# Kernel optimization log

Measured on AMD Instinct MI355X. Metric: run time of the kernel, lower is better.

## Reference

```python
import jax, jax.numpy as jnp
import numpy as np

BN_EPS = 1e-5

def setup_inputs() -> dict:
    key = jax.random.key(0)
    ks = jax.random.split(key, 8)
    N, E, D = 50000, 800000, 128
    x = jax.random.normal(ks[0], (N, D), dtype=jnp.float32)
    edge_index = jax.random.randint(ks[1], (2, E), 0, N, dtype=jnp.int64)
    s = 1.0 / np.sqrt(D)
    W1 = jax.random.uniform(ks[2], (D, D), jnp.float32, -s, s)
    b1 = jax.random.uniform(ks[3], (D,), jnp.float32, -s, s)
    W2 = jax.random.uniform(ks[4], (D, D), jnp.float32, -s, s)
    b2 = jax.random.uniform(ks[5], (D,), jnp.float32, -s, s)
    g1 = jnp.ones((D,), jnp.float32); be1 = jnp.zeros((D,), jnp.float32)
    g2 = jnp.ones((D,), jnp.float32); be2 = jnp.zeros((D,), jnp.float32)
    eps = jnp.zeros((), jnp.float32)  # learnable GIN epsilon (train_eps=True)
    return {"x": x, "edge_index": edge_index, "eps": eps,
            "W1": W1, "b1": b1, "g1": g1, "be1": be1,
            "W2": W2, "b2": b2, "g2": g2, "be2": be2}

def _batchnorm(h, gamma, beta):
    # training-mode BatchNorm1d over node axis (biased variance)
    mu = jnp.mean(h, axis=0)
    var = jnp.mean(jnp.square(h - mu), axis=0)
    return (h - mu) * jax.lax.rsqrt(var + BN_EPS) * gamma + beta

def reference(x, edge_index, eps, W1, b1, g1, be1, W2, b2, g2, be2):
    N = x.shape[0]
    src, dst = edge_index[0], edge_index[1]
    # GIN aggregation: sum of neighbor features (scatter-add to target nodes)
    agg = jax.ops.segment_sum(x[src], dst, num_segments=N)  # [N, D]
    h = (1.0 + eps) * x + agg
    # MLP: Linear -> BN -> ReLU -> Linear
    h = h @ W1.T + b1
    h = jax.nn.relu(_batchnorm(h, g1, be1))
    h = h @ W2.T + b2
    # outer BatchNorm + ReLU
    return jax.nn.relu(_batchnorm(h, g2, be2))
```

## Files before the change

### kernel.cpp

```cpp
#include <hip/hip_runtime.h>
#include <hip/hip_bf16.h>


#define DIM 128
#define SUB 2
#define CAP 32
#define KMAX 64
#define RBLK 2048

typedef unsigned short u16;
typedef __attribute__((ext_vector_type(8))) short short8;
typedef __attribute__((ext_vector_type(8))) unsigned short ushort8;
typedef __attribute__((ext_vector_type(4))) float f32x4;

__device__ inline u16 f2b(float f) {
  unsigned int u = __builtin_bit_cast(unsigned int, f);
  u += 0x7fffu + ((u >> 16) & 1u);
  return (u16)(u >> 16);
}
__device__ inline float b2f(u16 b) {
  unsigned int u = ((unsigned int)b) << 16;
  return __builtin_bit_cast(float, u);
}

__global__ __launch_bounds__(256) void prep_reorder_kernel(
    const float* __restrict__ W1, const float* __restrict__ W2,
    const float* __restrict__ x, const int* __restrict__ ei,
    int* __restrict__ cursor, u16* __restrict__ buckets,
    u16* __restrict__ wb1, u16* __restrict__ wb2, u16* __restrict__ xb,
    int E, float p8N, int CT, int perC) {
  const int bid = blockIdx.x;
  const int phase = (bid >> 3) & 1;

#pragma unroll
  for (int ph = 0; ph < 2; ++ph) {
    if ((ph ^ phase) == 0) {
      const int beg = bid * perC;
      const int end = min(CT, beg + perC);
      for (int i = beg + (int)threadIdx.x; i < end; i += 256) {
        if (i < 4096) {
          const float4 v = reinterpret_cast<const float4*>(W1)[i];
          ushort4 o = {f2b(v.x), f2b(v.y), f2b(v.z), f2b(v.w)};
          reinterpret_cast<ushort4*>(wb1)[i] = o;
        } else if (i < 8192) {
          const int j = i - 4096;
          const float4 v = reinterpret_cast<const float4*>(W2)[j];
          ushort4 o = {f2b(v.x), f2b(v.y), f2b(v.z), f2b(v.w)};
          reinterpret_cast<ushort4*>(wb2)[j] = o;
        } else {
          const int j = i - 8192;
          const float4 v = reinterpret_cast<const float4*>(x)[j];
          ushort4 o = {f2b(v.x), f2b(v.y), f2b(v.z), f2b(v.w)};
          reinterpret_cast<ushort4*>(xb)[j] = o;
        }
      }
    } else {
      const int part = bid & 7;
      const int slice = bid >> 3;
      const int perE = (E + 255) >> 8;
      const int beg = slice * perE;
      const int end = min(E, beg + perE);
      const int way = threadIdx.x & 1;
      for (int e = beg + (int)threadIdx.x; e < end; e += 256) {
        const int d = ei[E + e];
        int p = (int)((float)d * p8N);
        if (p > 7) p = 7;
        if (p != part) continue;
        const int s = ei[e];
        const int pos = atomicAdd(&cursor[d * SUB + way], 1);
        if (pos < CAP) buckets[d * KMAX + way * CAP + pos] = (u16)s;
      }
    }
  }
}

__global__ __launch_bounds__(256) void aggregate_kernel(
    const u16* __restrict__ xb, const int* __restrict__ cursor,
    const u16* __restrict__ buckets, const float* __restrict__ epsp,
    u16* __restrict__ hb, int N) {
  const int wid = threadIdx.x >> 6;
  const int lane = threadIdx.x & 63;
  const int node = blockIdx.x * 4 + wid;
  if (node >= N) return;
  const int slot = lane >> 4;
  const int chunk = lane & 15;
  int c0 = cursor[node * SUB + 0]; if (c0 > CAP) c0 = CAP;
  int c1 = cursor[node * SUB + 1]; if (c1 > CAP) c1 = CAP;
  const int deg = c0 + c1;
  const u16* bk = buckets + node * KMAX;

  int my = 0;
  if (lane < c0) my = bk[lane];
  else if (lane - c0 < c1) my = bk[CAP + lane - c0];

  float acc[8];
#pragma unroll
  for (int f = 0; f < 8; ++f) acc[f] = 0.f;

  for (int t0 = 0; t0 < deg; t0 += 4) {
    const int idx = t0 + slot;
    const int src = __shfl(my, idx);
    const ushort8 v = *reinterpret_cast<const ushort8*>(xb + (size_t)src * DIM + chunk * 8);
    if (idx < deg) {
#pragma unroll
      for (int f = 0; f < 8; ++f) acc[f] += b2f(v[f]);
    }
  }
#pragma unroll
  for (int f = 0; f < 8; ++f) {
    acc[f] += __shfl_xor(acc[f], 16);
    acc[f] += __shfl_xor(acc[f], 32);
  }
  if (slot == 0) {
    const float k = 1.0f + epsp[0];
    const ushort8 xv = *reinterpret_cast<const ushort8*>(xb + (size_t)node * DIM + chunk * 8);
    ushort8 o;
#pragma unroll
    for (int f = 0; f < 8; ++f) o[f] = f2b(acc[f] + k * b2f(xv[f]));
    *reinterpret_cast<ushort8*>(hb + (size_t)node * DIM + chunk * 8) = o;
  }
}

template <int FUSE>
__global__ __launch_bounds__(256) void gemm_mfma_kernel(
    const void* __restrict__ Av, const u16* __restrict__ Wb,
    const float* __restrict__ bias, const float* __restrict__ statsIn,
    const float* __restrict__ gamma, const float* __restrict__ beta,
    void* __restrict__ Cv, float* __restrict__ statsOut, int N, float Ninv) {
  __shared__ float sred[4][DIM];
  __shared__ float qred[4][DIM];
  __shared__ float ssc[DIM];
  __shared__ float ssh[DIM];
  if (FUSE) {
    const int t = threadIdx.x;
    if (t < DIM) {
      const float mu = statsIn[t] * Ninv;
      const float var = statsIn[DIM + t] * Ninv - mu * mu;
      const float sc = gamma[t] * rsqrtf(var + 1e-5f);
      ssc[t] = sc;
      ssh[t] = beta[t] - mu * sc;
    }
    __syncthreads();
  }
  const int lane = threadIdx.x & 63;
  const int wid = threadIdx.x >> 6;
  const int l15 = lane & 15;
  const int lg = lane >> 4;
  const int wrow = blockIdx.x * 64 + wid * 16;

  f32x4 acc[8];
#pragma unroll
  for (int ni = 0; ni < 8; ++ni) acc[ni] = (f32x4){0.f, 0.f, 0.f, 0.f};

  int arow = wrow + l15;
  if (arow >= N) arow = N - 1;

#pragma unroll
  for (int kb = 0; kb < 4; ++kb) {
    const int k0 = kb * 32 + lg * 8;
    short8 a;
    if (FUSE) {
      const float* A = (const float*)Av + (size_t)arow * DIM + k0;
      const float4 v0 = *reinterpret_cast<const float4*>(A);
      const float4 v1 = *reinterpret_cast<const float4*>(A + 4);
      a[0] = (short)f2b(fmaxf(fmaf(v0.x, ssc[k0 + 0], ssh[k0 + 0]), 0.f));
      a[1] = (short)f2b(fmaxf(fmaf(v0.y, ssc[k0 + 1], ssh[k0 + 1]), 0.f));
      a[2] = (short)f2b(fmaxf(fmaf(v0.z, ssc[k0 + 2], ssh[k0 + 2]), 0.f));
      a[3] = (short)f2b(fmaxf(fmaf(v0.w, ssc[k0 + 3], ssh[k0 + 3]), 0.f));
      a[4] = (short)f2b(fmaxf(fmaf(v1.x, ssc[k0 + 4], ssh[k0 + 4]), 0.f));
      a[5] = (short)f2b(fmaxf(fmaf(v1.y, ssc[k0 + 5], ssh[k0 + 5]), 0.f));
      a[6] = (short)f2b(fmaxf(fmaf(v1.z, ssc[k0 + 6], ssh[k0 + 6]), 0.f));
      a[7] = (short)f2b(fmaxf(fmaf(v1.w, ssc[k0 + 7], ssh[k0 + 7]), 0.f));
    } else {
      a = *reinterpret_cast<const short8*>((const u16*)Av + (size_t)arow * DIM + k0);
    }
#pragma unroll
    for (int ni = 0; ni < 8; ++ni) {
      const short8 b = *reinterpret_cast<const short8*>(Wb + (ni * 16 + l15) * DIM + k0);
      acc[ni] = __builtin_amdgcn_mfma_f32_16x16x32_bf16(a, b, acc[ni], 0, 0, 0);
    }
  }

  const int rbase = wrow + lg * 4;
#pragma unroll
  for (int ni = 0; ni < 8; ++ni) {
    const int col = ni * 16 + l15;
    const float bv = bias[col];
    float s = 0.f, q = 0.f;
#pragma unroll
    for (int r = 0; r < 4; ++r) {
      const int row = rbase + r;
      if (row < N) {
        const float v = acc[ni][r] + bv;
        if (FUSE) {
          const u16 bb = f2b(v);
          const float vr = b2f(bb);
          ((u16*)Cv)[(size_t)row * DIM + col] = bb;
          s += vr;
          q = fmaf(vr, vr, q);
        } else {
          ((float*)Cv)[(size_t)row * DIM + col] = v;
          s += v;
          q = fmaf(v, v, q);
        }
      }
    }
    s += __shfl_xor(s, 16); s += __shfl_xor(s, 32);
    q += __shfl_xor(q, 16); q += __shfl_xor(q, 32);
    if (lg == 0) { sred[wid][col] = s; qred[wid][col] = q; }
  }
  __syncthreads();
  const int t = threadIdx.x;
  if (t < DIM) {
    unsafeAtomicAdd(&statsOut[t], sred[0][t] + sred[1][t] + sred[2][t] + sred[3][t]);
  } else {
    const int c = t - DIM;
    unsafeAtomicAdd(&statsOut[DIM + c], qred[0][c] + qred[1][c] + qred[2][c] + qred[3][c]);
  }
}

__global__ __launch_bounds__(256) void bnrelu_kernel(
    const u16* __restrict__ hb, float* __restrict__ out,
    const float* __restrict__ stats, const float* __restrict__ gamma,
    const float* __restrict__ beta, float Ninv, int total8) {
  __shared__ float ssc[DIM];
  __shared__ float ssh[DIM];
  {
    const int t = threadIdx.x;
    if (t < DIM) {
      const float mu = stats[t] * Ninv;
      const float var = stats[DIM + t] * Ninv - mu * mu;
      const float sc = gamma[t] * rsqrtf(var + 1e-5f);
      ssc[t] = sc;
      ssh[t] = beta[t] - mu * sc;
    }
    __syncthreads();
  }
  int i = blockIdx.x * blockDim.x + threadIdx.x;
  const int stride = gridDim.x * blockDim.x;
  for (; i < total8; i += stride) {
    const int c0 = (i * 8) & (DIM - 1);
    const ushort8 v = reinterpret_cast<const ushort8*>(hb)[i];
    float4 o0, o1;
    o0.x = fmaxf(fmaf(b2f(v[0]), ssc[c0 + 0], ssh[c0 + 0]), 0.f);
    o0.y = fmaxf(fmaf(b2f(v[1]), ssc[c0 + 1], ssh[c0 + 1]), 0.f);
    o0.z = fmaxf(fmaf(b2f(v[2]), ssc[c0 + 2], ssh[c0 + 2]), 0.f);
    o0.w = fmaxf(fmaf(b2f(v[3]), ssc[c0 + 3], ssh[c0 + 3]), 0.f);
    o1.x = fmaxf(fmaf(b2f(v[4]), ssc[c0 + 4], ssh[c0 + 4]), 0.f);
    o1.y = fmaxf(fmaf(b2f(v[5]), ssc[c0 + 5], ssh[c0 + 5]), 0.f);
    o1.z = fmaxf(fmaf(b2f(v[6]), ssc[c0 + 6], ssh[c0 + 6]), 0.f);
    o1.w = fmaxf(fmaf(b2f(v[7]), ssc[c0 + 7], ssh[c0 + 7]), 0.f);
    reinterpret_cast<float4*>(out)[i * 2] = o0;
    reinterpret_cast<float4*>(out)[i * 2 + 1] = o1;
  }
}

extern "C" void kernel_launch(void* const* d_in, const int* in_sizes, int n_in,
                              void* d_out, int out_size, void* d_ws, size_t ws_size,
                              hipStream_t stream) {
  const float* x   = (const float*)d_in[0];
  const int*   ei  = (const int*)d_in[1];
  const float* eps = (const float*)d_in[2];
  const float* W1  = (const float*)d_in[3];
  const float* b1  = (const float*)d_in[4];
  const float* g1  = (const float*)d_in[5];
  const float* be1 = (const float*)d_in[6];
  const float* W2  = (const float*)d_in[7];
  const float* b2  = (const float*)d_in[8];
  const float* g2  = (const float*)d_in[9];
  const float* be2 = (const float*)d_in[10];
  float* out = (float*)d_out;

  const int N = in_sizes[0] / DIM;
  const int E = in_sizes[1] / 2;

  u16* hb      = (u16*)d_ws;
  u16* wb1     = hb + (size_t)N * DIM;
  u16* wb2     = wb1 + DIM * DIM;
  u16* buckets = wb2 + DIM * DIM;
  int* cursor  = (int*)(buckets + (size_t)N * KMAX);
  float* stats1 = (float*)(cursor + SUB * N);
  float* stats2 = stats1 + 256;

  u16* xb = (u16*)d_out;

  const int NX = N * DIM / 4;
  const int CT = 8192 + NX;
  const int perC = (CT + RBLK - 1) / RBLK;
  const float Ninv = 1.0f / N;
  const float p8N = 8.0f / N;

  hipMemsetAsync(cursor, 0, (size_t)(SUB * N + 512) * sizeof(int), stream);

  prep_reorder_kernel<<<RBLK, 256, 0, stream>>>(
      W1, W2, x, ei, cursor, buckets, wb1, wb2, xb, E, p8N, CT, perC);

  aggregate_kernel<<<(N + 3) / 4, 256, 0, stream>>>(xb, cursor, buckets, eps, hb, N);

  const int gblocks = (N + 63) / 64;
  gemm_mfma_kernel<0><<<gblocks, 256, 0, stream>>>(
      hb, wb1, b1, nullptr, nullptr, nullptr, (float*)d_out, stats1, N, Ninv);
  gemm_mfma_kernel<1><<<gblocks, 256, 0, stream>>>(
      (float*)d_out, wb2, b2, stats1, g1, be1, hb, stats2, N, Ninv);
  bnrelu_kernel<<<2048, 256, 0, stream>>>(hb, out, stats2, g2, be2, Ninv, N * (DIM / 8));
}
```

Before: 253.8 us.

## Apply W1 before aggregation and overlap first GEMM with edge bucketing

Uses linearity to compute y = x·W1ᵀ first (fused with the x-to-bf16 conversion) and then aggregates y over neighbours, adding bias afterward. This removes the separate x conversion pass and the first GEMM over the aggregated features. The y GEMM blocks share a launch with the edge-bucketing blocks so the two overlap. A separate stats kernel now reads h1 to compute BN1 statistics, and cursor zeroing moves from a memset into a setup kernel. The gather loop is unrolled to two rows per iteration, and nontemporal loads and stores are added. This adds an extra full read of h1 and changes bf16 rounding points.

```diff
diff --git a/kernel.cpp b/kernel.cpp
--- a/kernel.cpp
+++ b/kernel.cpp
@@ -23,61 +23,100 @@
   return __builtin_bit_cast(float, u);
 }
 
-__global__ __launch_bounds__(256) void prep_reorder_kernel(
+__global__ __launch_bounds__(256) void setup_kernel(
     const float* __restrict__ W1, const float* __restrict__ W2,
-    const float* __restrict__ x, const int* __restrict__ ei,
-    int* __restrict__ cursor, u16* __restrict__ buckets,
-    u16* __restrict__ wb1, u16* __restrict__ wb2, u16* __restrict__ xb,
-    int E, float p8N, int CT, int perC) {
+    int* __restrict__ cursor, u16* __restrict__ wb1, u16* __restrict__ wb2, int ZC) {
+  int i = blockIdx.x * 256 + threadIdx.x;
+  const int stride = gridDim.x * 256;
+  const int e1 = ZC + 4096, e2 = ZC + 8192;
+  for (; i < e2; i += stride) {
+    if (i < ZC) {
+      int4 z = {0, 0, 0, 0};
+      reinterpret_cast<int4*>(cursor)[i] = z;
+    } else if (i < e1) {
+      const int j = i - ZC;
+      const float4 v = reinterpret_cast<const float4*>(W1)[j];
+      ushort4 o = {f2b(v.x), f2b(v.y), f2b(v.z), f2b(v.w)};
+      reinterpret_cast<ushort4*>(wb1)[j] = o;
+    } else {
+      const int j = i - e1;
+      const float4 v = reinterpret_cast<const float4*>(W2)[j];
+      ushort4 o = {f2b(v.x), f2b(v.y), f2b(v.z), f2b(v.w)};
+      reinterpret_cast<ushort4*>(wb2)[j] = o;
+    }
+  }
+}
+
+__global__ __launch_bounds__(256) void reorder_gemmy_kernel(
+    const float* __restrict__ x, const int* __restrict__ ei, const u16* __restrict__ wb1,
+    int* __restrict__ cursor, u16* __restrict__ buckets, u16* __restrict__ yb,
+    int E, float p8N, int N, int GB) {
   const int bid = blockIdx.x;
-  const int phase = (bid >> 3) & 1;
-
-#pragma unroll
-  for (int ph = 0; ph < 2; ++ph) {
-    if ((ph ^ phase) == 0) {
-      const int beg = bid * perC;
-      const int end = min(CT, beg + perC);
-      for (int i = beg + (int)threadIdx.x; i < end; i += 256) {
-        if (i < 4096) {
-          const float4 v = reinterpret_cast<const float4*>(W1)[i];
-          ushort4 o = {f2b(v.x), f2b(v.y), f2b(v.z), f2b(v.w)};
-          reinterpret_cast<ushort4*>(wb1)[i] = o;
-        } else if (i < 8192) {
-          const int j = i - 4096;
-          const float4 v = reinterpret_cast<const float4*>(W2)[j];
-          ushort4 o = {f2b(v.x), f2b(v.y), f2b(v.z), f2b(v.w)};
-          reinterpret_cast<ushort4*>(wb2)[j] = o;
-        } else {
-          const int j = i - 8192;
-          const float4 v = reinterpret_cast<const float4*>(x)[j];
-          ushort4 o = {f2b(v.x), f2b(v.y), f2b(v.z), f2b(v.w)};
-          reinterpret_cast<ushort4*>(xb)[j] = o;
-        }
+  if (bid < GB) {
+    const int lane = threadIdx.x & 63;
+    const int wid = threadIdx.x >> 6;
+    const int l15 = lane & 15;
+    const int lg = lane >> 4;
+    const int wrow = bid * 64 + wid * 16;
+
+    f32x4 acc[8];
+#pragma unroll
+    for (int ni = 0; ni < 8; ++ni) acc[ni] = (f32x4){0.f, 0.f, 0.f, 0.f};
+
+    int arow = wrow + l15;
+    if (arow >= N) arow = N - 1;
+
+#pragma unroll
+    for (int kb = 0; kb < 4; ++kb) {
+      const int k0 = kb * 32 + lg * 8;
+      const f32x4* A = reinterpret_cast<const f32x4*>(x + (size_t)arow * DIM + k0);
+      const f32x4 v0 = __builtin_nontemporal_load(A);
+      const f32x4 v1 = __builtin_nontemporal_load(A + 1);
+      short8 a;
+      a[0] = (short)f2b(v0.x); a[1] = (short)f2b(v0.y);
+      a[2] = (short)f2b(v0.z); a[3] = (short)f2b(v0.w);
+      a[4] = (short)f2b(v1.x); a[5] = (short)f2b(v1.y);
+      a[6] = (short)f2b(v1.z); a[7] = (short)f2b(v1.w);
+#pragma unroll
+      for (int ni = 0; ni < 8; ++ni) {
+        const short8 b = *reinterpret_cast<const short8*>(wb1 + (ni * 16 + l15) * DIM + k0);
+        acc[ni] = __builtin_amdgcn_mfma_f32_16x16x32_bf16(a, b, acc[ni], 0, 0, 0);
       }
-    } else {
-      const int part = bid & 7;
-      const int slice = bid >> 3;
-      const int perE = (E + 255) >> 8;
-      const int beg = slice * perE;
-      const int end = min(E, beg + perE);
-      const int way = threadIdx.x & 1;
-      for (int e = beg + (int)threadIdx.x; e < end; e += 256) {
-        const int d = ei[E + e];
-        int p = (int)((float)d * p8N);
-        if (p > 7) p = 7;
-        if (p != part) continue;
-        const int s = ei[e];
-        const int pos = atomicAdd(&cursor[d * SUB + way], 1);
-        if (pos < CAP) buckets[d * KMAX + way * CAP + pos] = (u16)s;
+    }
+    const int rbase = wrow + lg * 4;
+#pragma unroll
+    for (int ni = 0; ni < 8; ++ni) {
+      const int col = ni * 16 + l15;
+#pragma unroll
+      for (int r = 0; r < 4; ++r) {
+        const int row = rbase + r;
+        if (row < N) yb[(size_t)row * DIM + col] = f2b(acc[ni][r]);
       }
     }
+  } else {
+    const int rb = bid - GB;
+    const int part = rb & 7;
+    const int slice = rb >> 3;
+    const int perE = (E + 255) >> 8;
+    const int beg = slice * perE;
+    const int end = min(E, beg + perE);
+    const int way = threadIdx.x & 1;
+    for (int e = beg + (int)threadIdx.x; e < end; e += 256) {
+      const int d = __builtin_nontemporal_load(ei + E + e);
+      int p = (int)((float)d * p8N);
+      if (p > 7) p = 7;
+      if (p != part) continue;
+      const int s = __builtin_nontemporal_load(ei + e);
+      const int pos = atomicAdd(&cursor[d * SUB + way], 1);
+      if (pos < CAP) buckets[d * KMAX + way * CAP + pos] = (u16)s;
+    }
   }
 }
 
 __global__ __launch_bounds__(256) void aggregate_kernel(
-    const u16* __restrict__ xb, const int* __restrict__ cursor,
+    const u16* __restrict__ yb, const int* __restrict__ cursor,
     const u16* __restrict__ buckets, const float* __restrict__ epsp,
-    u16* __restrict__ hb, int N) {
+    const float* __restrict__ b1, float* __restrict__ h1, int N) {
   const int wid = threadIdx.x >> 6;
   const int lane = threadIdx.x & 63;
   const int node = blockIdx.x * 4 + wid;
@@ -97,13 +136,20 @@
 #pragma unroll
   for (int f = 0; f < 8; ++f) acc[f] = 0.f;
 
-  for (int t0 = 0; t0 < deg; t0 += 4) {
-    const int idx = t0 + slot;
-    const int src = __shfl(my, idx);
-    const ushort8 v = *reinterpret_cast<const ushort8*>(xb + (size_t)src * DIM + chunk * 8);
-    if (idx < deg) {
-#pragma unroll
-      for (int f = 0; f < 8; ++f) acc[f] += b2f(v[f]);
+  for (int t0 = 0; t0 < deg; t0 += 8) {
+    const int i1 = t0 + slot;
+    const int i2 = t0 + 4 + slot;
+    const int s1 = __shfl(my, i1);
+    const int s2 = __shfl(my, i2);
+    const ushort8 v1 = *reinterpret_cast<const ushort8*>(yb + (size_t)s1 * DIM + chunk * 8);
+    const ushort8 v2 = *reinterpret_cast<const ushort8*>(yb + (size_t)s2 * DIM + chunk * 8);
+    if (i1 < deg) {
+#pragma unroll
+      for (int f = 0; f < 8; ++f) acc[f] += b2f(v1[f]);
+    }
+    if (i2 < deg) {
+#pragma unroll
+      for (int f = 0; f < 8; ++f) acc[f] += b2f(v2[f]);
     }
   }
 #pragma unroll
@@ -113,25 +159,54 @@
   }
   if (slot == 0) {
     const float k = 1.0f + epsp[0];
-    const ushort8 xv = *reinterpret_cast<const ushort8*>(xb + (size_t)node * DIM + chunk * 8);
-    ushort8 o;
-#pragma unroll
-    for (int f = 0; f < 8; ++f) o[f] = f2b(acc[f] + k * b2f(xv[f]));
-    *reinterpret_cast<ushort8*>(hb + (size_t)node * DIM + chunk * 8) = o;
-  }
-}
-
-template <int FUSE>
-__global__ __launch_bounds__(256) void gemm_mfma_kernel(
-    const void* __restrict__ Av, const u16* __restrict__ Wb,
+    const ushort8 xv = *reinterpret_cast<const ushort8*>(yb + (size_t)node * DIM + chunk * 8);
+    const float4 bb0 = *reinterpret_cast<const float4*>(b1 + chunk * 8);
+    const float4 bb1 = *reinterpret_cast<const float4*>(b1 + chunk * 8 + 4);
+    float4 o0, o1;
+    o0.x = acc[0] + k * b2f(xv[0]) + bb0.x;
+    o0.y = acc[1] + k * b2f(xv[1]) + bb0.y;
+    o0.z = acc[2] + k * b2f(xv[2]) + bb0.z;
+    o0.w = acc[3] + k * b2f(xv[3]) + bb0.w;
+    o1.x = acc[4] + k * b2f(xv[4]) + bb1.x;
+    o1.y = acc[5] + k * b2f(xv[5]) + bb1.y;
+    o1.z = acc[6] + k * b2f(xv[6]) + bb1.z;
+    o1.w = acc[7] + k * b2f(xv[7]) + bb1.w;
+    float4* dst = reinterpret_cast<float4*>(h1 + (size_t)node * DIM + chunk * 8);
+    dst[0] = o0;
+    dst[1] = o1;
+  }
+}
+
+__global__ __launch_bounds__(256) void stats_kernel(
+    const float* __restrict__ H, float* __restrict__ stats, int N) {
+  __shared__ float red[256];
+  const int col = threadIdx.x & 127;
+  const int sub = threadIdx.x >> 7;
+  float s = 0.f, sq = 0.f;
+  for (int row = blockIdx.x * 2 + sub; row < N; row += gridDim.x * 2) {
+    const float v = H[(size_t)row * DIM + col];
+    s += v;
+    sq = fmaf(v, v, sq);
+  }
+  red[threadIdx.x] = s;
+  __syncthreads();
+  if (sub == 0) unsafeAtomicAdd(&stats[col], s + red[threadIdx.x + 128]);
+  __syncthreads();
+  red[threadIdx.x] = sq;
+  __syncthreads();
+  if (sub == 0) unsafeAtomicAdd(&stats[DIM + col], sq + red[threadIdx.x + 128]);
+}
+
+__global__ __launch_bounds__(256) void gemm2_kernel(
+    const float* __restrict__ A, const u16* __restrict__ Wb,
     const float* __restrict__ bias, const float* __restrict__ statsIn,
     const float* __restrict__ gamma, const float* __restrict__ beta,
-    void* __restrict__ Cv, float* __restrict__ statsOut, int N, float Ninv) {
+    u16* __restrict__ C, float* __restrict__ statsOut, int N, float Ninv) {
   __shared__ float sred[4][DIM];
   __shared__ float qred[4][DIM];
   __shared__ float ssc[DIM];
   __shared__ float ssh[DIM];
-  if (FUSE) {
+  {
     const int t = threadIdx.x;
     if (t < DIM) {
       const float mu = statsIn[t] * Ninv;
@@ -158,22 +233,18 @@
 #pragma unroll
   for (int kb = 0; kb < 4; ++kb) {
     const int k0 = kb * 32 + lg * 8;
+    const float* Ap = A + (size_t)arow * DIM + k0;
+    const float4 v0 = *reinterpret_cast<const float4*>(Ap);
+    const float4 v1 = *reinterpret_cast<const float4*>(Ap + 4);
     short8 a;
-    if (FUSE) {
-      const float* A = (const float*)Av + (size_t)arow * DIM + k0;
-      const float4 v0 = *reinterpret_cast<const float4*>(A);
-      const float4 v1 = *reinterpret_cast<const float4*>(A + 4);
-      a[0] = (short)f2b(fmaxf(fmaf(v0.x, ssc[k0 + 0], ssh[k0 + 0]), 0.f));
-      a[1] = (short)f2b(fmaxf(fmaf(v0.y, ssc[k0 + 1], ssh[k0 + 1]), 0.f));
-      a[2] = (short)f2b(fmaxf(fmaf(v0.z, ssc[k0 + 2], ssh[k0 + 2]), 0.f));
-      a[3] = (short)f2b(fmaxf(fmaf(v0.w, ssc[k0 + 3], ssh[k0 + 3]), 0.f));
-      a[4] = (short)f2b(fmaxf(fmaf(v1.x, ssc[k0 + 4], ssh[k0 + 4]), 0.f));
-      a[5] = (short)f2b(fmaxf(fmaf(v1.y, ssc[k0 + 5], ssh[k0 + 5]), 0.f));
-      a[6] = (short)f2b(fmaxf(fmaf(v1.z, ssc[k0 + 6], ssh[k0 + 6]), 0.f));
-      a[7] = (short)f2b(fmaxf(fmaf(v1.w, ssc[k0 + 7], ssh[k0 + 7]), 0.f));
-    } else {
-      a = *reinterpret_cast<const short8*>((const u16*)Av + (size_t)arow * DIM + k0);
-    }
+    a[0] = (short)f2b(fmaxf(fmaf(v0.x, ssc[k0 + 0], ssh[k0 + 0]), 0.f));
+    a[1] = (short)f2b(fmaxf(fmaf(v0.y, ssc[k0 + 1], ssh[k0 + 1]), 0.f));
+    a[2] = (short)f2b(fmaxf(fmaf(v0.z, ssc[k0 + 2], ssh[k0 + 2]), 0.f));
+    a[3] = (short)f2b(fmaxf(fmaf(v0.w, ssc[k0 + 3], ssh[k0 + 3]), 0.f));
+    a[4] = (short)f2b(fmaxf(fmaf(v1.x, ssc[k0 + 4], ssh[k0 + 4]), 0.f));
+    a[5] = (short)f2b(fmaxf(fmaf(v1.y, ssc[k0 + 5], ssh[k0 + 5]), 0.f));
+    a[6] = (short)f2b(fmaxf(fmaf(v1.z, ssc[k0 + 6], ssh[k0 + 6]), 0.f));
+    a[7] = (short)f2b(fmaxf(fmaf(v1.w, ssc[k0 + 7], ssh[k0 + 7]), 0.f));
 #pragma unroll
     for (int ni = 0; ni < 8; ++ni) {
       const short8 b = *reinterpret_cast<const short8*>(Wb + (ni * 16 + l15) * DIM + k0);
@@ -192,17 +263,11 @@
       const int row = rbase + r;
       if (row < N) {
         const float v = acc[ni][r] + bv;
-        if (FUSE) {
-          const u16 bb = f2b(v);
-          const float vr = b2f(bb);
-          ((u16*)Cv)[(size_t)row * DIM + col] = bb;
-          s += vr;
-          q = fmaf(vr, vr, q);
-        } else {
-          ((float*)Cv)[(size_t)row * DIM + col] = v;
-          s += v;
-          q = fmaf(v, v, q);
-        }
+        const u16 bb = f2b(v);
+        const float vr = b2f(bb);
+        C[(size_t)row * DIM + col] = bb;
+        s += vr;
+        q = fmaf(vr, vr, q);
       }
     }
     s += __shfl_xor(s, 16); s += __shfl_xor(s, 32);
@@ -241,7 +306,7 @@
   for (; i < total8; i += stride) {
     const int c0 = (i * 8) & (DIM - 1);
     const ushort8 v = reinterpret_cast<const ushort8*>(hb)[i];
-    float4 o0, o1;
+    f32x4 o0, o1;
     o0.x = fmaxf(fmaf(b2f(v[0]), ssc[c0 + 0], ssh[c0 + 0]), 0.f);
     o0.y = fmaxf(fmaf(b2f(v[1]), ssc[c0 + 1], ssh[c0 + 1]), 0.f);
     o0.z = fmaxf(fmaf(b2f(v[2]), ssc[c0 + 2], ssh[c0 + 2]), 0.f);
@@ -250,8 +315,8 @@
     o1.y = fmaxf(fmaf(b2f(v[5]), ssc[c0 + 5], ssh[c0 + 5]), 0.f);
     o1.z = fmaxf(fmaf(b2f(v[6]), ssc[c0 + 6], ssh[c0 + 6]), 0.f);
     o1.w = fmaxf(fmaf(b2f(v[7]), ssc[c0 + 7], ssh[c0 + 7]), 0.f);
-    reinterpret_cast<float4*>(out)[i * 2] = o0;
-    reinterpret_cast<float4*>(out)[i * 2 + 1] = o1;
+    __builtin_nontemporal_store(o0, reinterpret_cast<f32x4*>(out) + i * 2);
+    __builtin_nontemporal_store(o1, reinterpret_cast<f32x4*>(out) + i * 2 + 1);
   }
 }
 
@@ -274,33 +339,26 @@
   const int N = in_sizes[0] / DIM;
   const int E = in_sizes[1] / 2;
 
-  u16* hb      = (u16*)d_ws;
-  u16* wb1     = hb + (size_t)N * DIM;
+  u16* yb      = (u16*)d_ws;
+  u16* wb1     = yb + (size_t)N * DIM;
   u16* wb2     = wb1 + DIM * DIM;
   u16* buckets = wb2 + DIM * DIM;
   int* cursor  = (int*)(buckets + (size_t)N * KMAX);
   float* stats1 = (float*)(cursor + SUB * N);
   float* stats2 = stats1 + 256;
 
-  u16* xb = (u16*)d_out;
-
-  const int NX = N * DIM / 4;
-  const int CT = 8192 + NX;
-  const int perC = (CT + RBLK - 1) / RBLK;
+  float* h1 = (float*)d_out;
+
+  const int ZC = (SUB * N + 512 + 3) / 4;
   const float Ninv = 1.0f / N;
   const float p8N = 8.0f / N;
-
-  hipMemsetAsync(cursor, 0, (size_t)(SUB * N + 512) * sizeof(int), stream);
-
-  prep_reorder_kernel<<<RBLK, 256, 0, stream>>>(
-      W1, W2, x, ei, cursor, buckets, wb1, wb2, xb, E, p8N, CT, perC);
-
-  aggregate_kernel<<<(N + 3) / 4, 256, 0, stream>>>(xb, cursor, buckets, eps, hb, N);
-
-  const int gblocks = (N + 63) / 64;
-  gemm_mfma_kernel<0><<<gblocks, 256, 0, stream>>>(
-      hb, wb1, b1, nullptr, nullptr, nullptr, (float*)d_out, stats1, N, Ninv);
-  gemm_mfma_kernel<1><<<gblocks, 256, 0, stream>>>(
-      (float*)d_out, wb2, b2, stats1, g1, be1, hb, stats2, N, Ninv);
-  bnrelu_kernel<<<2048, 256, 0, stream>>>(hb, out, stats2, g2, be2, Ninv, N * (DIM / 8));
-}
+  const int GB = (N + 63) / 64;
+
+  setup_kernel<<<132, 256, 0, stream>>>(W1, W2, cursor, wb1, wb2, ZC);
+  reorder_gemmy_kernel<<<GB + RBLK, 256, 0, stream>>>(
+      x, ei, wb1, cursor, buckets, yb, E, p8N, N, GB);
+  aggregate_kernel<<<(N + 3) / 4, 256, 0, stream>>>(yb, cursor, buckets, eps, b1, h1, N);
+  stats_kernel<<<512, 256, 0, stream>>>(h1, stats1, N);
+  gemm2_kernel<<<GB, 256, 0, stream>>>(h1, wb2, b2, stats1, g1, be1, yb, stats2, N, Ninv);
+  bnrelu_kernel<<<2048, 256, 0, stream>>>(yb, out, stats2, g2, be2, Ninv, N * (DIM / 8));
+}
```

Result: slower. 277.0 us (+9.1%).
